# Kernel optimization log

Hardware: AMD Instinct MI355X
Metric: run time of the kernel (lower is better)

## Reference

```python
import jax, jax.numpy as jnp
from jax import lax
import numpy as np

CONF_THRESH = 0.015
NMS_DIST = 4
BORDER = 4
RED = 8


def setup_inputs() -> dict:
    key = jax.random.key(0)
    k1, k2, k3, k4, k5 = jax.random.split(key, 5)
    B, C, H, W = 32, 128, 64, 64
    MID, NCLS = 256, RED * RED + 1
    return {
        "x": jax.random.normal(k1, (B, C, H, W), dtype=jnp.float32),
        "w1": jax.random.normal(k2, (MID, C, 3, 3), dtype=jnp.float32) * 0.05,
        "b1": jax.random.normal(k3, (MID,), dtype=jnp.float32) * 0.05,
        "w2": jax.random.normal(k4, (NCLS, MID, 1, 1), dtype=jnp.float32) * 0.05,
        "b2": jax.random.normal(k5, (NCLS,), dtype=jnp.float32) * 0.05,
    }


def _conv3x3(x, w, b):
    y = lax.conv_general_dilated(
        x, w, window_strides=(1, 1), padding="SAME",
        dimension_numbers=("NCHW", "OIHW", "NCHW"))
    return y + b[None, :, None, None]


def _max_pool(s, r):
    # s: [B, H, W]; infinity-norm neighborhood max, window (2r+1)x(2r+1)
    return lax.reduce_window(
        s, -jnp.inf, lax.max,
        window_dimensions=(1, 2 * r + 1, 2 * r + 1),
        window_strides=(1, 1, 1), padding="SAME")


def _grid_nms(scores, r, iters=8):
    # Iterated local-max suppression; converges to the greedy (sorted-by-score)
    # grid NMS of the original nms_fast routine for distinct scores.
    zeros = jnp.zeros_like(scores)
    max_mask = (scores == _max_pool(scores, r)) & (scores > 0)
    for _ in range(iters):
        supp = _max_pool(max_mask.astype(scores.dtype), r) > 0
        supp_scores = jnp.where(supp, zeros, scores)
        new_max = (supp_scores == _max_pool(supp_scores, r)) & (supp_scores > 0)
        max_mask = max_mask | (new_max & ~supp)
    return jnp.where(max_mask, scores, zeros)


def reference(x, w1, b1, w2, b2):
    B, _, hh, ww = x.shape
    h = jax.nn.relu(_conv3x3(x, w1, b1))                       # [B, mid, hh, ww]
    semi = jnp.einsum("bchw,oc->bohw", h, w2[:, :, 0, 0]) + b2[None, :, None, None]
    dense = jax.nn.softmax(semi, axis=1)                        # [B, 65, hh, ww]
    nodust = dense[:, :-1]                                      # drop dust bin
    # depth-to-space: [B,64,hh,ww] -> [B, hh*8, ww*8]
    heat = nodust.transpose(0, 2, 3, 1).reshape(B, hh, ww, RED, RED)
    heat = heat.transpose(0, 1, 3, 2, 4).reshape(B, hh * RED, ww * RED)
    # confidence threshold
    scores = jnp.where(heat >= CONF_THRESH, heat, 0.0)
    # grid-based NMS (dense keep-map formulation of nms_fast)
    kept = _grid_nms(scores, NMS_DIST)
    # border removal
    Hi, Wi = hh * RED, ww * RED
    yy = jnp.arange(Hi)
    xx = jnp.arange(Wi)
    border = ((yy[:, None] >= BORDER) & (yy[:, None] < Hi - BORDER) &
              (xx[None, :] >= BORDER) & (xx[None, :] < Wi - BORDER))
    return kept * border[None, :, :].astype(kept.dtype)
```

## Files before the change

### kernel.cpp

```cpp
#include <hip/hip_runtime.h>
#include <hip/hip_bf16.h>
#include <stdint.h>

#define BATCH 32
#define CIN 128
#define HH 64
#define WW 64
#define MID 256
#define NCLS 65
#define HI 512
#define NWORDS 8
#define HBS2 264
#define SEMS 68
#define RMS 68

typedef _Float16 half8 __attribute__((ext_vector_type(8)));
typedef _Float16 half4v __attribute__((ext_vector_type(4)));
typedef _Float16 half2v __attribute__((ext_vector_type(2)));
typedef float f32x4 __attribute__((ext_vector_type(4)));

__global__ __launch_bounds__(256) void prep_wf(
    const float* __restrict__ w1, const float* __restrict__ w2,
    _Float16* __restrict__ w1fh, _Float16* __restrict__ w1fl,
    _Float16* __restrict__ w2fh, _Float16* __restrict__ w2fl,
    int* __restrict__ flags)
{
    if (blockIdx.x == 0 && threadIdx.x < 16) flags[threadIdx.x] = 0;
    const int idx = blockIdx.x * 256 + threadIdx.x;
    if (idx < 294912) {
        const int j = idx & 7, lane = (idx >> 3) & 63, mt = (idx >> 9) & 15;
        const int s = (idx >> 13) & 3, kix = idx >> 15;
        const int m = mt * 16 + (lane & 15);
        const int c = s * 32 + (lane >> 4) * 8 + j;
        const int ky = kix / 3, kx = kix - ky * 3;
        const float v = w1[((m * CIN + c) * 3 + ky) * 3 + kx];
        const _Float16 hi = (_Float16)v;
        w1fh[idx] = hi;
        w1fl[idx] = (_Float16)(v - (float)hi);
    } else {
        const int i2 = idx - 294912;
        const int j = i2 & 7, lane = (i2 >> 3) & 63;
        const int ks = (i2 >> 9) & 7, mt = i2 >> 12;
        const int o = mt * 16 + (lane & 15);
        const int k = ks * 32 + (lane >> 4) * 8 + j;
        const float v = (o < NCLS) ? w2[o * MID + k] : 0.f;
        const _Float16 hi = (_Float16)v;
        w2fh[i2] = hi;
        w2fl[i2] = (_Float16)(v - (float)hi);
    }
}

__global__ __launch_bounds__(256, 4) void head_kernel(
    const float* __restrict__ x,
    const _Float16* __restrict__ w1fh, const _Float16* __restrict__ w1fl,
    const _Float16* __restrict__ w2fh, const _Float16* __restrict__ w2fl,
    const float* __restrict__ b1, const float* __restrict__ b2,
    float* __restrict__ out)
{
    const int b  = blockIdx.z;
    const int y0 = blockIdx.y * 8, x0 = blockIdx.x * 8;
    const int tid = threadIdx.x;
    const int lane = tid & 63, w = tid >> 6;
    const int n = lane & 15, q = lane >> 4;

    __shared__ __align__(16) unsigned char SM[25600];
    char* const xhb = (char*)SM;
    _Float16* const hbh = (_Float16*)SM;
    _Float16* const hbl = hbh + 16 * HBS2;
    float* const sem  = (float*)(SM + 16896);
    float* const rinv = sem + 16 * SEMS;

    f32x4 acc[4][4];
#pragma unroll
    for (int i = 0; i < 4; ++i)
#pragma unroll
        for (int t = 0; t < 4; ++t) acc[i][t] = (f32x4){0.f, 0.f, 0.f, 0.f};

    int bposT[4];
#pragma unroll
    for (int t = 0; t < 4; ++t)
        bposT[t] = (t * 2 + (n >> 3)) * 10 + (n & 7);

    const float* xb = x + (size_t)b * CIN * HH * WW;

    for (int half = 0; half < 2; ++half) {
        if (half) __syncthreads();
        for (int i = tid; i < 3200; i += 256) {
            const int c2h = i / 100, pos = i - c2h * 100;
            const int r = pos / 10, cc = pos - r * 10;
            const int gy = y0 - 1 + r, gx = x0 - 1 + cc;
            float v0 = 0.f, v1 = 0.f;
            if ((unsigned)gy < HH && (unsigned)gx < WW) {
                const float* p =
                    xb + (((half * 32 + c2h) * 2) * HH + gy) * WW + gx;
                v0 = p[0]; v1 = p[HH * WW];
            }
            const _Float16 h0 = (_Float16)v0, h1 = (_Float16)v1;
            half2v hi = {h0, h1};
            half2v lo = {(_Float16)(v0 - (float)h0),
                         (_Float16)(v1 - (float)h1)};
            const int slot = (c2h >> 2) ^ (pos & 7);
            char* p16 = xhb + pos * 128 + (slot << 4) + (c2h & 3) * 4;
            *(half2v*)p16 = hi;
            *(half2v*)(p16 + 12800) = lo;
        }
        __syncthreads();

        for (int kix = 0; kix < 9; ++kix) {
            const int ky = kix / 3;
            const int koff = ky * 10 + (kix - ky * 3);
#pragma unroll
            for (int sl = 0; sl < 2; ++sl) {
                half8 Bh[4], Bl[4];
#pragma unroll
                for (int t = 0; t < 4; ++t) {
                    const int pos = bposT[t] + koff;
                    const int byteoff = pos * 128 +
                        ((((sl << 2) + q) ^ (pos & 7)) << 4);
                    Bh[t] = *(const half8*)(xhb + byteoff);
                    Bl[t] = *(const half8*)(xhb + 12800 + byteoff);
                }
                const int s = half * 2 + sl;
#pragma unroll
                for (int i = 0; i < 4; ++i) {
                    const size_t o = (size_t)(kix * 4 + s) * 8192 +
                                     (w * 4 + i) * 512 + lane * 8;
                    const half8 Ah = *(const half8*)(w1fh + o);
                    const half8 Al = *(const half8*)(w1fl + o);
#pragma unroll
                    for (int t = 0; t < 4; ++t) {
                        acc[i][t] = __builtin_amdgcn_mfma_f32_16x16x32_f16(
                            Ah, Bh[t], acc[i][t], 0, 0, 0);
                        acc[i][t] = __builtin_amdgcn_mfma_f32_16x16x32_f16(
                            Ah, Bl[t], acc[i][t], 0, 0, 0);
                        acc[i][t] = __builtin_amdgcn_mfma_f32_16x16x32_f16(
                            Al, Bh[t], acc[i][t], 0, 0, 0);
                    }
                }
            }
        }
    }
    __syncthreads();

#pragma unroll
    for (int qt = 0; qt < 4; ++qt) {
        if (qt) __syncthreads();
#pragma unroll
        for (int i = 0; i < 4; ++i) {
            const int m0 = w * 64 + i * 16 + q * 4;
            const f32x4 a = acc[i][qt];
            const float4 bv = *(const float4*)(b1 + m0);
            const float h0 = fmaxf(a[0] + bv.x, 0.f);
            const float h1 = fmaxf(a[1] + bv.y, 0.f);
            const float h2 = fmaxf(a[2] + bv.z, 0.f);
            const float h3 = fmaxf(a[3] + bv.w, 0.f);
            half4v hh = {(_Float16)h0, (_Float16)h1,
                         (_Float16)h2, (_Float16)h3};
            half4v hl = {(_Float16)(h0 - (float)hh[0]),
                         (_Float16)(h1 - (float)hh[1]),
                         (_Float16)(h2 - (float)hh[2]),
                         (_Float16)(h3 - (float)hh[3])};
            *(half4v*)(hbh + n * HBS2 + m0) = hh;
            *(half4v*)(hbl + n * HBS2 + m0) = hl;
        }
        __syncthreads();
        {
            const int extra = qt & 3;
            f32x4 a2[2];
            a2[0] = (f32x4){0.f, 0.f, 0.f, 0.f};
            a2[1] = (f32x4){0.f, 0.f, 0.f, 0.f};
#pragma unroll
            for (int ks = 0; ks < 8; ++ks) {
                const int ad = n * HBS2 + ks * 32 + q * 8;
                const half8 B2h = *(const half8*)(hbh + ad);
                const half8 B2l = *(const half8*)(hbl + ad);
                {
                    const size_t o = (size_t)(w * 8 + ks) * 512 + lane * 8;
                    const half8 A2h = *(const half8*)(w2fh + o);
                    const half8 A2l = *(const half8*)(w2fl + o);
                    a2[0] = __builtin_amdgcn_mfma_f32_16x16x32_f16(
                        A2h, B2h, a2[0], 0, 0, 0);
                    a2[0] = __builtin_amdgcn_mfma_f32_16x16x32_f16(
                        A2h, B2l, a2[0], 0, 0, 0);
                    a2[0] = __builtin_amdgcn_mfma_f32_16x16x32_f16(
                        A2l, B2h, a2[0], 0, 0, 0);
                }
                if (w == extra) {
                    const size_t o = (size_t)(4 * 8 + ks) * 512 + lane * 8;
                    const half8 A2h = *(const half8*)(w2fh + o);
                    const half8 A2l = *(const half8*)(w2fl + o);
                    a2[1] = __builtin_amdgcn_mfma_f32_16x16x32_f16(
                        A2h, B2h, a2[1], 0, 0, 0);
                    a2[1] = __builtin_amdgcn_mfma_f32_16x16x32_f16(
                        A2h, B2l, a2[1], 0, 0, 0);
                    a2[1] = __builtin_amdgcn_mfma_f32_16x16x32_f16(
                        A2l, B2h, a2[1], 0, 0, 0);
                }
            }
#pragma unroll
            for (int r2 = 0; r2 < 4; ++r2) {
                const int o = w * 16 + q * 4 + r2;
                sem[n * SEMS + o] = a2[0][r2] + b2[o];
            }
            if (w == extra && q == 0)
                sem[n * SEMS + 64] = a2[1][0] + b2[64];
        }
        __syncthreads();
        if (tid < 64) {
            const int p = tid >> 2, q4 = tid & 3;
            const int o0 = q4 * 17;
            const int o1 = (o0 + 17 < NCLS) ? o0 + 17 : NCLS;
            float mx = -1e30f;
            for (int o = o0; o < o1; ++o)
                mx = fmaxf(mx, sem[p * SEMS + o]);
            mx = fmaxf(mx, __shfl_xor(mx, 1));
            mx = fmaxf(mx, __shfl_xor(mx, 2));
            float ssum = 0.f;
            for (int o = o0; o < o1; ++o) {
                float e = __expf(sem[p * SEMS + o] - mx);
                sem[p * SEMS + o] = e;
                ssum += e;
            }
            ssum += __shfl_xor(ssum, 1);
            ssum += __shfl_xor(ssum, 2);
            if (q4 == 0) rinv[p] = 1.f / ssum;
        }
        __syncthreads();
        for (int t2 = tid; t2 < 1024; t2 += 256) {
            const int p = t2 >> 6, o = t2 & 63;
            float v = sem[p * SEMS + o] * rinv[p];
            if (!(v >= 0.015f)) v = 0.f;
            const int P = qt * 16 + p;
            const int py = P >> 3, px = P & 7;
            const int row = (y0 + py) * 8 + (o >> 3);
            const int col = (x0 + px) * 8 + (o & 7);
            out[((size_t)b * HI + row) * HI + col] = v;
        }
    }
}

__device__ __forceinline__ void nms_hmax_phase(
    const float* __restrict__ Sb, const uint64_t* __restrict__ sup,
    float* __restrict__ rm, int ty, int tx, int tid, int rbase)
{
    const int lane = tid & 63;
    for (int k = tid; k < 640; k += 256) {
        const int rr = k >> 4, g = k & 15;
        const int r = rbase + rr;
        const int gy = ty - 4 + r;
        const int x4 = g * 4;
        const uint64_t* sr = sup + r * 3;
        float own[4] = {0.f, 0.f, 0.f, 0.f};
        float halo[4] = {0.f, 0.f, 0.f, 0.f};
        if ((unsigned)gy < HI) {
            const float* row = Sb + (size_t)gy * HI;
            const float4 o4 = *(const float4*)(row + tx + x4);
            own[0] = o4.x; own[1] = o4.y; own[2] = o4.z; own[3] = o4.w;
            const uint64_t w1 = sr[1];
#pragma unroll
            for (int cc = 0; cc < 4; ++cc)
                if ((w1 >> (x4 + cc)) & 1ull) own[cc] = 0.f;
            if (g == 0 && tx >= 4) {
                const float4 h4 = *(const float4*)(row + tx - 4);
                halo[0] = h4.x; halo[1] = h4.y; halo[2] = h4.z; halo[3] = h4.w;
                const uint64_t w0 = sr[0];
#pragma unroll
                for (int cc = 0; cc < 4; ++cc)
                    if ((w0 >> (60 + cc)) & 1ull) halo[cc] = 0.f;
            } else if (g == 15 && tx + 64 < HI) {
                const float4 h4 = *(const float4*)(row + tx + 64);
                halo[0] = h4.x; halo[1] = h4.y; halo[2] = h4.z; halo[3] = h4.w;
                const uint64_t w2 = sr[2];
#pragma unroll
                for (int cc = 0; cc < 4; ++cc)
                    if ((w2 >> cc) & 1ull) halo[cc] = 0.f;
            }
        }
        float v[12];
#pragma unroll
        for (int cc = 0; cc < 4; ++cc) {
            v[4 + cc] = own[cc];
            v[cc]     = __shfl(own[cc], lane - 1);
            v[8 + cc] = __shfl(own[cc], lane + 1);
        }
        if (g == 0) {
#pragma unroll
            for (int cc = 0; cc < 4; ++cc) v[cc] = halo[cc];
        } else if (g == 15) {
#pragma unroll
            for (int cc = 0; cc < 4; ++cc) v[8 + cc] = halo[cc];
        }
        const float m4567 = fmaxf(fmaxf(v[4],v[5]), fmaxf(v[6],v[7]));
        const float m23 = fmaxf(v[2],v[3]), m89 = fmaxf(v[8],v[9]);
        const float o0 = fmaxf(fmaxf(fmaxf(v[0],v[1]), m23),
                               fmaxf(m4567, v[8]));
        const float o1 = fmaxf(fmaxf(v[1], m23), fmaxf(m4567, m89));
        const float o2 = fmaxf(fmaxf(m23, m4567), fmaxf(m89, v[10]));
        const float o3 = fmaxf(fmaxf(v[3], m4567),
                               fmaxf(fmaxf(m89, v[10]), v[11]));
        *(float4*)(rm + rr * RMS + x4) = make_float4(o0,o1,o2,o3);
    }
}

__global__ __launch_bounds__(256, 8) void nms_iter(
    const float* __restrict__ S, const uint64_t* __restrict__ Min,
    uint64_t* __restrict__ Mout, int* __restrict__ flags, int chk, int set)
{
    const int b = blockIdx.z;
    const int bx = blockIdx.x;
    const int ty = blockIdx.y * 64, tx = bx * 64;
    const int tid = threadIdx.x;

    if (chk >= 0 && flags[chk] == 0) {
        for (int y = tid; y < 64; y += 256)
            Mout[((size_t)b * HI + ty + y) * NWORDS + bx] =
                Min[((size_t)b * HI + ty + y) * NWORDS + bx];
        return;
    }

    __shared__ uint64_t smw[80 * 3];
    __shared__ uint64_t hd[80 * 3];
    __shared__ uint64_t sup[72 * 3];
    __shared__ __align__(16) float rm[40 * RMS];

    const float* Sb = S + (size_t)b * HI * HI;
    int chg = 0;

    if (Min) {
        if (tid < 240) {
            const int i = tid / 3, j = tid % 3;
            const int yy = ty - 8 + i;
            const int wj = bx - 1 + j;
            uint64_t v = 0;
            if ((unsigned)yy < HI && (unsigned)wj < NWORDS)
                v = Min[((size_t)b * HI + yy) * NWORDS + wj];
            smw[tid] = v;
        }
        __syncthreads();
        if (tid < 240) {
            const int j = tid % 3;
            const uint64_t c = smw[tid];
            const uint64_t l = j > 0 ? smw[tid - 1] : 0ull;
            const uint64_t r = j < 2 ? smw[tid + 1] : 0ull;
            uint64_t d = c;
#pragma unroll
            for (int s = 1; s <= 4; ++s)
                d |= (c >> s) | (r << (64 - s)) | (c << s) | (l >> (64 - s));
            hd[tid] = d;
        }
        __syncthreads();
        if (tid < 216) {
            uint64_t v = 0;
#pragma unroll
            for (int k = 0; k < 9; ++k) v |= hd[tid + 3 * k];
            sup[tid] = v;
        }
        __syncthreads();
    } else {
        if (tid < 240) smw[tid] = 0;
        if (tid < 216) sup[tid] = 0;
        __syncthreads();
    }

    for (int half = 0; half < 2; ++half) {
        const int rbase = half * 32;
        nms_hmax_phase(Sb, sup, rm, ty, tx, tid, rbase);
        __syncthreads();
        {
            const int wv = tid >> 6, lane = tid & 63;
            const int rb = wv * 8;
            const int ybase = rbase + rb;
            float ring[9];
#pragma unroll
            for (int k = 0; k < 8; ++k) ring[k] = rm[(rb + k) * RMS + lane];
#pragma unroll
            for (int qq = 0; qq < 8; ++qq) {
                const int y = ybase + qq;
                ring[(qq + 8) % 9] = rm[(rb + qq + 8) * RMS + lane];
                float mv = ring[0];
#pragma unroll
                for (int k = 1; k < 9; ++k) mv = fmaxf(mv, ring[k]);
                float c = Sb[(size_t)(ty + y) * HI + tx + lane];
                if ((sup[(y + 4) * 3 + 1] >> lane) & 1ull) c = 0.f;
                const uint64_t oldw = smw[(y + 8) * 3 + 1];
                const bool keep = ((oldw >> lane) & 1ull) ||
                                  (c > 0.f && c == mv);
                const uint64_t word = __ballot(keep);
                if (lane == 0) {
                    Mout[((size_t)b * HI + ty + y) * NWORDS + bx] = word;
                    if (word != oldw) chg = 1;
                }
            }
        }
        __syncthreads();
    }
    if (set >= 0 && (tid & 63) == 0 && chg) flags[set] = 1;
}

__global__ __launch_bounds__(256, 8) void nms_last(
    const float* __restrict__ S, const uint64_t* __restrict__ Min,
    float* __restrict__ out, const int* __restrict__ flags)
{
    const int b = blockIdx.z;
    const int bx = blockIdx.x;
    const int ty = blockIdx.y * 64, tx = bx * 64;
    const int tid = threadIdx.x;

    const float* Sb = S + (size_t)b * HI * HI;

    if (flags[7] == 0) {
        for (int k = tid; k < 1024; k += 256) {
            const int r = k >> 4, c4 = k & 15;
            const int gy = ty + r;
            const int gx0 = tx + c4 * 4;
            const uint64_t w = Min[((size_t)b * HI + gy) * NWORDS + bx];
            float4 v = *(const float4*)(Sb + (size_t)gy * HI + gx0);
            float* pv = (float*)&v;
            const bool rowok = (gy >= 4) && (gy < HI - 4);
#pragma unroll
            for (int cc = 0; cc < 4; ++cc) {
                const int xx = gx0 + cc;
                const bool keep = rowok && (xx >= 4) && (xx < HI - 4) &&
                                  ((w >> ((c4 * 4 + cc) & 63)) & 1ull);
                if (!keep) pv[cc] = 0.f;
            }
            *(float4*)(out + ((size_t)b * HI + gy) * HI + gx0) = v;
        }
        return;
    }

    __shared__ uint64_t smw[80 * 3];
    __shared__ uint64_t hd[80 * 3];
    __shared__ uint64_t sup[72 * 3];
    __shared__ __align__(16) float rm[40 * RMS];

    if (tid < 240) {
        const int i = tid / 3, j = tid % 3;
        const int yy = ty - 8 + i;
        const int wj = bx - 1 + j;
        uint64_t v = 0;
        if ((unsigned)yy < HI && (unsigned)wj < NWORDS)
            v = Min[((size_t)b * HI + yy) * NWORDS + wj];
        smw[tid] = v;
    }
    __syncthreads();
    if (tid < 240) {
        const int j = tid % 3;
        const uint64_t c = smw[tid];
        const uint64_t l = j > 0 ? smw[tid - 1] : 0ull;
        const uint64_t r = j < 2 ? smw[tid + 1] : 0ull;
        uint64_t d = c;
#pragma unroll
        for (int s = 1; s <= 4; ++s)
            d |= (c >> s) | (r << (64 - s)) | (c << s) | (l >> (64 - s));
        hd[tid] = d;
    }
    __syncthreads();
    if (tid < 216) {
        uint64_t v = 0;
#pragma unroll
        for (int k = 0; k < 9; ++k) v |= hd[tid + 3 * k];
        sup[tid] = v;
    }
    __syncthreads();

    for (int half = 0; half < 2; ++half) {
        const int rbase = half * 32;
        nms_hmax_phase(Sb, sup, rm, ty, tx, tid, rbase);
        __syncthreads();
        {
            const int wv = tid >> 6, lane = tid & 63;
            const int rb = wv * 8;
            const int ybase = rbase + rb;
            float ring[9];
#pragma unroll
            for (int k = 0; k < 8; ++k) ring[k] = rm[(rb + k) * RMS + lane];
#pragma unroll
            for (int qq = 0; qq < 8; ++qq) {
                const int y = ybase + qq;
                ring[(qq + 8) % 9] = rm[(rb + qq + 8) * RMS + lane];
                float mv = ring[0];
#pragma unroll
                for (int k = 1; k < 9; ++k) mv = fmaxf(mv, ring[k]);
                const int gy = ty + y, gx = tx + lane;
                const float corig = Sb[(size_t)gy * HI + gx];
                float c = corig;
                if ((sup[(y + 4) * 3 + 1] >> lane) & 1ull) c = 0.f;
                const uint64_t oldw = smw[(y + 8) * 3 + 1];
                const bool keep = ((oldw >> lane) & 1ull) ||
                                  (c > 0.f && c == mv);
                const bool border = (gy >= 4) && (gy < HI - 4) &&
                                    (gx >= 4) && (gx < HI - 4);
                out[((size_t)b * HI + gy) * HI + gx] =
                    (keep && border) ? corig : 0.f;
            }
        }
        __syncthreads();
    }
}

__global__ __launch_bounds__(256) void finalize_bits(
    float* __restrict__ S, const uint64_t* __restrict__ Mw)
{
    const int i4 = blockIdx.x * 256 + threadIdx.x;
    const size_t base = (size_t)i4 * 4;
    const int x = (int)(base & 511);
    const int y = (int)((base >> 9) & 511);
    const int bb = (int)(base >> 18);
    const uint64_t w = Mw[((size_t)bb * HI + y) * NWORDS + (x >> 6)];
    float4 v = ((const float4*)S)[i4];
    float* pv = (float*)&v;
    const bool rowok = (y >= 4) && (y < HI - 4);
#pragma unroll
    for (int cc = 0; cc < 4; ++cc) {
        const int xx = x + cc;
        const bool keep = rowok && (xx >= 4) && (xx < HI - 4) &&
                          ((w >> (xx & 63)) & 1ull);
        if (!keep) pv[cc] = 0.f;
    }
    ((float4*)S)[i4] = v;
}

extern "C" void kernel_launch(void* const* d_in, const int* in_sizes, int n_in,
                              void* d_out, int out_size, void* d_ws, size_t ws_size,
                              hipStream_t stream) {
    const float* x  = (const float*)d_in[0];
    const float* w1 = (const float*)d_in[1];
    const float* b1 = (const float*)d_in[2];
    const float* w2 = (const float*)d_in[3];
    const float* b2 = (const float*)d_in[4];
    float* out = (float*)d_out;

    char* wsb = (char*)d_ws;
    _Float16* w1fh = (_Float16*)(wsb);
    _Float16* w1fl = (_Float16*)(wsb + 0x90000);
    _Float16* w2fh = (_Float16*)(wsb + 0x120000);
    _Float16* w2fl = (_Float16*)(wsb + 0x130000);
    int* flags     = (int*)(wsb + 0x13B000);
    uint64_t* MA   = (uint64_t*)(wsb + 0x140000);
    uint64_t* MB   = (uint64_t*)(wsb + 0x240000);

    const size_t S_OFF = 0x340000;
    const size_t S_BYTES = (size_t)BATCH * HI * HI * 4;
    const bool use_ws = ws_size >= S_OFF + S_BYTES;
    float* S = use_ws ? (float*)(wsb + S_OFF) : out;

    prep_wf<<<1232, 256, 0, stream>>>(w1, w2, w1fh, w1fl, w2fh, w2fl, flags);
    head_kernel<<<dim3(8, 8, BATCH), 256, 0, stream>>>(
        x, w1fh, w1fl, w2fh, w2fl, b1, b2, S);

    dim3 g(NWORDS, 8, BATCH);
    nms_iter<<<g, 256, 0, stream>>>(S, nullptr, MA, flags, -1, -1);
    nms_iter<<<g, 256, 0, stream>>>(S, MA, MB, flags, -1, 1);
    nms_iter<<<g, 256, 0, stream>>>(S, MB, MA, flags, 1, 2);
    nms_iter<<<g, 256, 0, stream>>>(S, MA, MB, flags, 2, 3);
    nms_iter<<<g, 256, 0, stream>>>(S, MB, MA, flags, 3, 4);
    nms_iter<<<g, 256, 0, stream>>>(S, MA, MB, flags, 4, 5);
    nms_iter<<<g, 256, 0, stream>>>(S, MB, MA, flags, 5, 6);
    nms_iter<<<g, 256, 0, stream>>>(S, MA, MB, flags, 6, 7);

    if (use_ws) {
        nms_last<<<g, 256, 0, stream>>>(S, MB, out, flags);
    } else {
        nms_iter<<<g, 256, 0, stream>>>(S, MB, MA, flags, 7, -1);
        const int nf4 = BATCH * HI * HI / 4;
        finalize_bits<<<nf4 / 256, 256, 0, stream>>>(out, MA);
    }
}
```

Measured before the change: 590.7 us.

## Split head kernel work across eight waves instead of four

Doubles the head kernel block to 512 threads, so each wave owns 32 of the 256 mid channels instead of 64. That halves per-wave accumulator registers and MFMA work. The 1x1 classifier stage is redistributed so that waves 0-4 each compute one 16-class tile, which removes the special extra-wave path for the dust class. Higher per-block thread count may reduce blocks per CU, and the B fragments are now loaded redundantly by twice as many waves.

```diff
diff --git a/kernel.cpp b/kernel.cpp
--- a/kernel.cpp
+++ b/kernel.cpp
@@ -50,7 +50,7 @@
     }
 }
 
-__global__ __launch_bounds__(256, 4) void head_kernel(
+__global__ __launch_bounds__(512, 4) void head_kernel(
     const float* __restrict__ x,
     const _Float16* __restrict__ w1fh, const _Float16* __restrict__ w1fl,
     const _Float16* __restrict__ w2fh, const _Float16* __restrict__ w2fl,
@@ -70,9 +70,9 @@
     float* const sem  = (float*)(SM + 16896);
     float* const rinv = sem + 16 * SEMS;
 
-    f32x4 acc[4][4];
-#pragma unroll
-    for (int i = 0; i < 4; ++i)
+    f32x4 acc[2][4];
+#pragma unroll
+    for (int i = 0; i < 2; ++i)
 #pragma unroll
         for (int t = 0; t < 4; ++t) acc[i][t] = (f32x4){0.f, 0.f, 0.f, 0.f};
 
@@ -85,7 +85,7 @@
 
     for (int half = 0; half < 2; ++half) {
         if (half) __syncthreads();
-        for (int i = tid; i < 3200; i += 256) {
+        for (int i = tid; i < 3200; i += 512) {
             const int c2h = i / 100, pos = i - c2h * 100;
             const int r = pos / 10, cc = pos - r * 10;
             const int gy = y0 - 1 + r, gx = x0 - 1 + cc;
@@ -122,9 +122,9 @@
                 }
                 const int s = half * 2 + sl;
 #pragma unroll
-                for (int i = 0; i < 4; ++i) {
+                for (int i = 0; i < 2; ++i) {
                     const size_t o = (size_t)(kix * 4 + s) * 8192 +
-                                     (w * 4 + i) * 512 + lane * 8;
+                                     (w * 2 + i) * 512 + lane * 8;
                     const half8 Ah = *(const half8*)(w1fh + o);
                     const half8 Al = *(const half8*)(w1fl + o);
 #pragma unroll
@@ -146,8 +146,8 @@
     for (int qt = 0; qt < 4; ++qt) {
         if (qt) __syncthreads();
 #pragma unroll
-        for (int i = 0; i < 4; ++i) {
-            const int m0 = w * 64 + i * 16 + q * 4;
+        for (int i = 0; i < 2; ++i) {
+            const int m0 = w * 32 + i * 16 + q * 4;
             const f32x4 a = acc[i][qt];
             const float4 bv = *(const float4*)(b1 + m0);
             const float h0 = fmaxf(a[0] + bv.x, 0.f);
@@ -164,46 +164,29 @@
             *(half4v*)(hbl + n * HBS2 + m0) = hl;
         }
         __syncthreads();
-        {
-            const int extra = qt & 3;
-            f32x4 a2[2];
-            a2[0] = (f32x4){0.f, 0.f, 0.f, 0.f};
-            a2[1] = (f32x4){0.f, 0.f, 0.f, 0.f};
+        if (w < 5) {
+            f32x4 a2 = (f32x4){0.f, 0.f, 0.f, 0.f};
 #pragma unroll
             for (int ks = 0; ks < 8; ++ks) {
                 const int ad = n * HBS2 + ks * 32 + q * 8;
                 const half8 B2h = *(const half8*)(hbh + ad);
                 const half8 B2l = *(const half8*)(hbl + ad);
-                {
-                    const size_t o = (size_t)(w * 8 + ks) * 512 + lane * 8;
-                    const half8 A2h = *(const half8*)(w2fh + o);
-                    const half8 A2l = *(const half8*)(w2fl + o);
-                    a2[0] = __builtin_amdgcn_mfma_f32_16x16x32_f16(
-                        A2h, B2h, a2[0], 0, 0, 0);
-                    a2[0] = __builtin_amdgcn_mfma_f32_16x16x32_f16(
-                        A2h, B2l, a2[0], 0, 0, 0);
-                    a2[0] = __builtin_amdgcn_mfma_f32_16x16x32_f16(
-                        A2l, B2h, a2[0], 0, 0, 0);
-                }
-                if (w == extra) {
-                    const size_t o = (size_t)(4 * 8 + ks) * 512 + lane * 8;
-                    const half8 A2h = *(const half8*)(w2fh + o);
-                    const half8 A2l = *(const half8*)(w2fl + o);
-                    a2[1] = __builtin_amdgcn_mfma_f32_16x16x32_f16(
-                        A2h, B2h, a2[1], 0, 0, 0);
-                    a2[1] = __builtin_amdgcn_mfma_f32_16x16x32_f16(
-                        A2h, B2l, a2[1], 0, 0, 0);
-                    a2[1] = __builtin_amdgcn_mfma_f32_16x16x32_f16(
-                        A2l, B2h, a2[1], 0, 0, 0);
-                }
+                const size_t o = (size_t)(w * 8 + ks) * 512 + lane * 8;
+                const half8 A2h = *(const half8*)(w2fh + o);
+                const half8 A2l = *(const half8*)(w2fl + o);
+                a2 = __builtin_amdgcn_mfma_f32_16x16x32_f16(
+                    A2h, B2h, a2, 0, 0, 0);
+                a2 = __builtin_amdgcn_mfma_f32_16x16x32_f16(
+                    A2h, B2l, a2, 0, 0, 0);
+                a2 = __builtin_amdgcn_mfma_f32_16x16x32_f16(
+                    A2l, B2h, a2, 0, 0, 0);
             }
 #pragma unroll
             for (int r2 = 0; r2 < 4; ++r2) {
                 const int o = w * 16 + q * 4 + r2;
-                sem[n * SEMS + o] = a2[0][r2] + b2[o];
-            }
-            if (w == extra && q == 0)
-                sem[n * SEMS + 64] = a2[1][0] + b2[64];
+                if (o < NCLS)
+                    sem[n * SEMS + o] = a2[r2] + b2[o];
+            }
         }
         __syncthreads();
         if (tid < 64) {
@@ -226,7 +209,7 @@
             if (q4 == 0) rinv[p] = 1.f / ssum;
         }
         __syncthreads();
-        for (int t2 = tid; t2 < 1024; t2 += 256) {
+        for (int t2 = tid; t2 < 1024; t2 += 512) {
             const int p = t2 >> 6, o = t2 & 63;
             float v = sem[p * SEMS + o] * rinv[p];
             if (!(v >= 0.015f)) v = 0.f;
@@ -546,7 +529,7 @@
     float* S = use_ws ? (float*)(wsb + S_OFF) : out;
 
     prep_wf<<<1232, 256, 0, stream>>>(w1, w2, w1fh, w1fl, w2fh, w2fl, flags);
-    head_kernel<<<dim3(8, 8, BATCH), 256, 0, stream>>>(
+    head_kernel<<<dim3(8, 8, BATCH), 512, 0, stream>>>(
         x, w1fh, w1fl, w2fh, w2fl, b1, b2, S);
 
     dim3 g(NWORDS, 8, BATCH);
```

Result: faster. 514.4 us (-12.9%).
